# Kernel tuning notes

Hardware: AMD Instinct MI355X
Metric: run time of the kernel (lower is better)

## Reference

```python
import jax, jax.numpy as jnp
import numpy as np

B, CIN, L = 16, 256, 2048
HID, G, M = 512, 2, 512
LP = L // 2  # pooled length == hidden_length of patterns
BETA = 1.0


def setup_inputs() -> dict:
    key = jax.random.key(0)
    k = jax.random.split(key, 6)
    x = jax.random.normal(k[0], (B, CIN, L), dtype=jnp.float32)
    # ChannelPool: Conv1d(256 -> 512, kernel=1, groups=2): weight [512, 128, 1]
    w1 = jax.random.normal(k[1], (HID, CIN // G, 1), dtype=jnp.float32) * 0.05
    b1 = jax.random.normal(k[2], (HID,), dtype=jnp.float32) * 0.01
    # StatePattern memory bank: [num_memories, hidden_length]
    patterns = jax.random.normal(k[3], (M, LP), dtype=jnp.float32) * 0.02
    # Unpool: ConvTranspose1d(512 -> 256, kernel=2, stride=2, groups=2):
    # torch weight layout [in_channels, out_channels//groups, kernel] = [512, 128, 2]
    wT = jax.random.normal(k[4], (HID, CIN // G, 2), dtype=jnp.float32) * 0.05
    bT = jax.random.normal(k[5], (CIN,), dtype=jnp.float32) * 0.01
    RZ = jnp.array(0.1, dtype=jnp.float32)
    return {"x": x, "w1": w1, "b1": b1, "patterns": patterns, "wT": wT, "bT": bT, "RZ": RZ}


def reference(x, w1, b1, patterns, wT, bT, RZ):
    identity = x
    # --- grouped 1x1 conv (ChannelPool) ---
    # split channels into G groups: x [B,G,CIN/G,L], w [G,HID/G,CIN/G]
    xg = x.reshape(B, G, CIN // G, L)
    wg = w1[:, :, 0].reshape(G, HID // G, CIN // G)
    h = jnp.einsum('bgil,goi->bgol', xg, wg).reshape(B, HID, L) + b1[None, :, None]
    h = jax.nn.relu(h)  # act; norm1/dropout are identity (norm=False, eval)
    # --- MaxPool1d(kernel=2, stride=2) ---
    h = h.reshape(B, HID, LP, 2).max(axis=-1)  # [B, HID, LP]
    # --- Hopfield retrieval: softmax(beta * x @ P^T) @ P ---
    scores = jnp.einsum('bcl,ml->bcm', BETA * h, patterns)  # [B, HID, M]
    attn = jax.nn.softmax(scores, axis=-1)
    h = jnp.einsum('bcm,ml->bcl', attn, patterns)  # [B, HID, LP]
    # --- grouped ConvTranspose1d(k=2, s=2) ---
    hg = h.reshape(B, G, HID // G, LP)
    wtg = wT.reshape(G, HID // G, CIN // G, 2)
    y = jnp.einsum('bgil,giok->bgolk', hg, wtg)  # [B,G,CIN/G,LP,2]
    y = y.reshape(B, CIN, L) + bT[None, :, None]
    y = jax.nn.relu(y)  # act; norm2/dropout identity
    return identity + RZ * y
```

## Files before the change

### kernel.cpp

```cpp
#include <hip/hip_runtime.h>

#define NB 16
#define NCIN 256
#define NL 2048
#define NHID 512
#define NM 512
#define NLP 1024
#define BK 64

typedef short bf16x8 __attribute__((ext_vector_type(8)));
typedef unsigned short u16x8 __attribute__((ext_vector_type(8)));
typedef float f32x4 __attribute__((ext_vector_type(4)));
typedef __attribute__((address_space(1))) const unsigned int gas_u32;
typedef __attribute__((address_space(3))) unsigned int las_u32;

__device__ __forceinline__ unsigned short f2bf(float f) {
    unsigned int u = __builtin_bit_cast(unsigned int, f);
    return (unsigned short)((u + 0x7FFFu + ((u >> 16) & 1u)) >> 16);
}
__device__ __forceinline__ float bf2f(unsigned short u) {
    return __builtin_bit_cast(float, ((unsigned int)u) << 16);
}

__global__ __launch_bounds__(256) void k_prep(
    const float* __restrict__ P, const float* __restrict__ w1,
    const float* __restrict__ wT, unsigned short* __restrict__ Pb,
    unsigned short* __restrict__ Ptb, unsigned short* __restrict__ w1b,
    unsigned short* __restrict__ wTt)
{
    __shared__ unsigned short tbuf[64][65];
    const int bb = blockIdx.x;
    if (bb < 128) {
        const int mt = bb >> 4;
        const int lt = bb & 15;
        for (int i = threadIdx.x; i < 4096; i += 256) {
            const int r = i >> 6, c = i & 63;
            const unsigned short b = f2bf(P[(size_t)(mt * 64 + r) * 1024 + lt * 64 + c]);
            Pb[(size_t)(mt * 64 + r) * 1024 + lt * 64 + c] = b;
            tbuf[c][r] = b;
        }
        __syncthreads();
        for (int i = threadIdx.x; i < 4096; i += 256) {
            const int r = i >> 6, c = i & 63;
            Ptb[(size_t)(lt * 64 + r) * 512 + mt * 64 + c] = tbuf[r][c];
        }
    } else {
        const int t = (bb - 128) * 256 + threadIdx.x;
        if (t < 65536) w1b[t] = f2bf(w1[t]);
        if (t < 131072) {
            const int g = t >> 16, ok = (t >> 8) & 255, i = t & 255;
            wTt[t] = f2bf(wT[((size_t)(g * 256 + i)) * 256 + ok]);
        }
    }
}

__global__ __launch_bounds__(256) void k0_xT(
    const float* __restrict__ x, unsigned short* __restrict__ xT)
{
    const int ct = blockIdx.x & 3;
    const int lt = (blockIdx.x >> 2) & 31;
    const int b  = blockIdx.x >> 7;
    __shared__ float tile[64 * 68];
    const int t = threadIdx.x;
    #pragma unroll
    for (int it = 0; it < 4; ++it) {
        const int idx = t + it * 256;
        const int ch = idx >> 4, f4 = idx & 15;
        const float4 v = *(const float4*)(x + ((size_t)(b * 256 + ct * 64 + ch)) * 2048 + lt * 64 + f4 * 4);
        *(float4*)(tile + ch * 68 + f4 * 4) = v;
    }
    __syncthreads();
    const int l = t >> 2, cq = t & 3;
    u16x8 o0, o1;
    #pragma unroll
    for (int k = 0; k < 8; ++k) o0[k] = f2bf(tile[(cq * 16 + k) * 68 + l]);
    #pragma unroll
    for (int k = 0; k < 8; ++k) o1[k] = f2bf(tile[(cq * 16 + 8 + k) * 68 + l]);
    unsigned short* dst = xT + ((size_t)(b * 2048 + lt * 64 + l)) * 256 + ct * 64 + cq * 16;
    *(u16x8*)dst = o0;
    *(u16x8*)(dst + 8) = o1;
}

__global__ __launch_bounds__(256) void k1_gemm(
    const unsigned short* __restrict__ xT, const unsigned short* __restrict__ w1b,
    const float* __restrict__ b1, unsigned short* __restrict__ h)
{
    const int nt = blockIdx.x & 1;
    const int g  = (blockIdx.x >> 1) & 1;
    const int rt = blockIdx.x >> 2;
    const int r0 = rt * 128;
    const int b  = r0 >> 11, l0 = r0 & 2047;
    const int c0 = g * 256 + nt * 128;

    __shared__ unsigned short Asl[128 * BK];
    __shared__ unsigned short Bsl[128 * BK];
    __shared__ unsigned short epi[128 * 72];

    const int t = threadIdx.x;
    const int lane = t & 63;
    const int wave = t >> 6;
    const int wm = wave & 1, wn = wave >> 1;
    const int q = lane >> 4, lm = lane & 15;

    f32x4 acc[4][4];
    #pragma unroll
    for (int i = 0; i < 4; ++i)
        #pragma unroll
        for (int j = 0; j < 4; ++j)
            #pragma unroll
            for (int r = 0; r < 4; ++r) acc[i][j][r] = 0.f;

    for (int k0 = 0; k0 < 128; k0 += BK) {
        #pragma unroll
        for (int rd = 0; rd < 4; ++rd) {
            const int e = rd * 2048 + t * 8;
            const int row = e >> 6, col = e & 63;
            const unsigned short* ga = xT + (size_t)(r0 + row) * 256 + g * 128 + k0 + col;
            __builtin_amdgcn_global_load_lds((gas_u32*)ga, (las_u32*)(Asl + e), 16, 0, 0);
            const unsigned short* gb = w1b + (size_t)(c0 + row) * 128 + k0 + col;
            __builtin_amdgcn_global_load_lds((gas_u32*)gb, (las_u32*)(Bsl + e), 16, 0, 0);
        }
        __syncthreads();
        #pragma unroll
        for (int kk = 0; kk < 2; ++kk) {
            bf16x8 af[4], bf[4];
            #pragma unroll
            for (int i = 0; i < 4; ++i)
                af[i] = *(const bf16x8*)(Asl + (wm * 64 + i * 16 + lm) * BK + kk * 32 + q * 8);
            #pragma unroll
            for (int j = 0; j < 4; ++j)
                bf[j] = *(const bf16x8*)(Bsl + (wn * 64 + j * 16 + lm) * BK + kk * 32 + q * 8);
            #pragma unroll
            for (int i = 0; i < 4; ++i)
                #pragma unroll
                for (int j = 0; j < 4; ++j)
                    acc[i][j] = __builtin_amdgcn_mfma_f32_16x16x32_bf16(af[i], bf[j], acc[i][j], 0, 0, 0);
        }
        __syncthreads();
    }

    #pragma unroll
    for (int j = 0; j < 4; ++j) {
        const int c_blk = wn * 64 + j * 16 + lm;
        const float bias = b1[c0 + c_blk];
        #pragma unroll
        for (int i = 0; i < 4; ++i) {
            const float p0 = fmaxf(fmaxf(acc[i][j][0], acc[i][j][1]) + bias, 0.f);
            const float p1 = fmaxf(fmaxf(acc[i][j][2], acc[i][j][3]) + bias, 0.f);
            const int lp_blk = wm * 32 + i * 8 + q * 2;
            ushort2 u; u.x = f2bf(p0); u.y = f2bf(p1);
            *(ushort2*)(epi + c_blk * 72 + lp_blk) = u;
        }
    }
    __syncthreads();
    const int c_blk = t >> 1, half = t & 1;
    unsigned short* dst = h + ((size_t)(b * 512 + c0 + c_blk)) * 1024 + (l0 >> 1) + half * 32;
    #pragma unroll
    for (int u = 0; u < 4; ++u)
        *(u16x8*)(dst + u * 8) = *(const u16x8*)(epi + c_blk * 72 + half * 32 + u * 8);
}

__global__ __launch_bounds__(512, 2) void gemm_sc(
    const unsigned short* __restrict__ A, const unsigned short* __restrict__ B,
    unsigned short* __restrict__ Sb)
{
    const int nt = blockIdx.x & 3;
    const int rt = blockIdx.x >> 2;
    const int r0 = rt * 128, n0 = nt * 128;

    __shared__ unsigned short Asl[128 * BK];
    __shared__ unsigned short Bsl[128 * BK];

    const int t = threadIdx.x;
    const int lane = t & 63;
    const int wave = t >> 6;
    const int wm = wave & 1, wn = wave >> 1;
    const int q = lane >> 4, lm = lane & 15;

    f32x4 acc[4][2];
    #pragma unroll
    for (int i = 0; i < 4; ++i)
        #pragma unroll
        for (int j = 0; j < 2; ++j)
            #pragma unroll
            for (int r = 0; r < 4; ++r) acc[i][j][r] = 0.f;

    for (int k0 = 0; k0 < 1024; k0 += BK) {
        #pragma unroll
        for (int rd = 0; rd < 2; ++rd) {
            const int e = rd * 4096 + t * 8;
            const int row = e >> 6, col = e & 63;
            const unsigned short* ga = A + (size_t)(r0 + row) * 1024 + k0 + col;
            __builtin_amdgcn_global_load_lds((gas_u32*)ga, (las_u32*)(Asl + e), 16, 0, 0);
            const unsigned short* gb = B + (size_t)(n0 + row) * 1024 + k0 + col;
            __builtin_amdgcn_global_load_lds((gas_u32*)gb, (las_u32*)(Bsl + e), 16, 0, 0);
        }
        __syncthreads();
        #pragma unroll
        for (int kk = 0; kk < 2; ++kk) {
            bf16x8 af[4], bf[2];
            #pragma unroll
            for (int i = 0; i < 4; ++i)
                af[i] = *(const bf16x8*)(Asl + (wm * 64 + i * 16 + lm) * BK + kk * 32 + q * 8);
            #pragma unroll
            for (int j = 0; j < 2; ++j)
                bf[j] = *(const bf16x8*)(Bsl + (wn * 32 + j * 16 + lm) * BK + kk * 32 + q * 8);
            #pragma unroll
            for (int i = 0; i < 4; ++i)
                #pragma unroll
                for (int j = 0; j < 2; ++j)
                    acc[i][j] = __builtin_amdgcn_mfma_f32_16x16x32_bf16(af[i], bf[j], acc[i][j], 0, 0, 0);
        }
        __syncthreads();
    }

    #pragma unroll
    for (int i = 0; i < 4; ++i)
        #pragma unroll
        for (int j = 0; j < 2; ++j)
            #pragma unroll
            for (int r = 0; r < 4; ++r)
                Sb[(size_t)(r0 + wm * 64 + i * 16 + q * 4 + r) * 512
                   + n0 + wn * 32 + j * 16 + lm] = f2bf(acc[i][j][r]);
}

__global__ __launch_bounds__(256) void k_softmax(
    const unsigned short* __restrict__ Sb, unsigned short* __restrict__ Ab)
{
    const int row = blockIdx.x * 4 + (threadIdx.x >> 6);
    const int lane = threadIdx.x & 63;
    const u16x8 uv = *(const u16x8*)(Sb + (size_t)row * 512 + lane * 8);

    float v[8];
    #pragma unroll
    for (int j = 0; j < 8; ++j) v[j] = bf2f(uv[j]);

    float mx = v[0];
    #pragma unroll
    for (int j = 1; j < 8; ++j) mx = fmaxf(mx, v[j]);
    for (int off = 32; off > 0; off >>= 1) mx = fmaxf(mx, __shfl_xor(mx, off));

    float sum = 0.f;
    #pragma unroll
    for (int j = 0; j < 8; ++j) { v[j] = __expf(v[j] - mx); sum += v[j]; }
    for (int off = 32; off > 0; off >>= 1) sum += __shfl_xor(sum, off);

    const float inv = 1.f / sum;
    u16x8 ov;
    #pragma unroll
    for (int j = 0; j < 8; ++j) ov[j] = f2bf(v[j] * inv);
    *(u16x8*)(Ab + (size_t)row * 512 + lane * 8) = ov;
}

__global__ __launch_bounds__(512, 4) void gemm_retr(
    const unsigned short* __restrict__ Ptb, const unsigned short* __restrict__ Ab,
    unsigned short* __restrict__ h2T)
{
    const int tl = blockIdx.x & 31;
    const int b  = blockIdx.x >> 5;
    const int nt = tl & 3;
    const int rt = tl >> 2;
    const int r0 = rt * 128, n0 = nt * 128;

    __shared__ unsigned short Asl[128 * BK];
    __shared__ unsigned short Bsl[128 * BK];

    const int t = threadIdx.x;
    const int lane = t & 63;
    const int wave = t >> 6;
    const int wm = wave & 1, wn = wave >> 1;
    const int q = lane >> 4, lm = lane & 15;

    f32x4 acc[4][2];
    #pragma unroll
    for (int i = 0; i < 4; ++i)
        #pragma unroll
        for (int j = 0; j < 2; ++j)
            #pragma unroll
            for (int r = 0; r < 4; ++r) acc[i][j][r] = 0.f;

    for (int k0 = 0; k0 < 512; k0 += BK) {
        #pragma unroll
        for (int rd = 0; rd < 2; ++rd) {
            const int e = rd * 4096 + t * 8;
            const int row = e >> 6, col = e & 63;
            const unsigned short* ga = Ptb + (size_t)(r0 + row) * 512 + k0 + col;
            __builtin_amdgcn_global_load_lds((gas_u32*)ga, (las_u32*)(Asl + e), 16, 0, 0);
            const unsigned short* gb = Ab + ((size_t)b * 512 + n0 + row) * 512 + k0 + col;
            __builtin_amdgcn_global_load_lds((gas_u32*)gb, (las_u32*)(Bsl + e), 16, 0, 0);
        }
        __syncthreads();
        #pragma unroll
        for (int kk = 0; kk < 2; ++kk) {
            bf16x8 af[4], bf[2];
            #pragma unroll
            for (int i = 0; i < 4; ++i)
                af[i] = *(const bf16x8*)(Asl + (wm * 64 + i * 16 + lm) * BK + kk * 32 + q * 8);
            #pragma unroll
            for (int j = 0; j < 2; ++j)
                bf[j] = *(const bf16x8*)(Bsl + (wn * 32 + j * 16 + lm) * BK + kk * 32 + q * 8);
            #pragma unroll
            for (int i = 0; i < 4; ++i)
                #pragma unroll
                for (int j = 0; j < 2; ++j)
                    acc[i][j] = __builtin_amdgcn_mfma_f32_16x16x32_bf16(af[i], bf[j], acc[i][j], 0, 0, 0);
        }
        __syncthreads();
    }

    #pragma unroll
    for (int i = 0; i < 4; ++i)
        #pragma unroll
        for (int j = 0; j < 2; ++j)
            #pragma unroll
            for (int r = 0; r < 4; ++r)
                h2T[((size_t)b * 1024 + r0 + wm * 64 + i * 16 + q * 4 + r) * 512
                    + n0 + wn * 32 + j * 16 + lm] = f2bf(acc[i][j][r]);
}

__global__ __launch_bounds__(256) void k4_gemm(
    const unsigned short* __restrict__ h2T, const unsigned short* __restrict__ wTt,
    const float* __restrict__ bT, const float* __restrict__ x,
    const float* __restrict__ RZ, float* __restrict__ out)
{
    const int nt = blockIdx.x & 1;
    const int g  = (blockIdx.x >> 1) & 1;
    const int rt = blockIdx.x >> 2;
    const int r0 = rt * 128;
    const int b  = r0 >> 10, lp0 = r0 & 1023;

    __shared__ __align__(16) char smem[65536];
    unsigned short* Asl = (unsigned short*)smem;
    unsigned short* Bsl = Asl + 128 * BK;
    float* epi = (float*)smem;

    const int t = threadIdx.x;
    const int lane = t & 63;
    const int wave = t >> 6;
    const int wm = wave & 1, wn = wave >> 1;
    const int q = lane >> 4, lm = lane & 15;

    f32x4 acc[4][4];
    #pragma unroll
    for (int i = 0; i < 4; ++i)
        #pragma unroll
        for (int j = 0; j < 4; ++j)
            #pragma unroll
            for (int r = 0; r < 4; ++r) acc[i][j][r] = 0.f;

    for (int k0 = 0; k0 < 256; k0 += BK) {
        #pragma unroll
        for (int rd = 0; rd < 4; ++rd) {
            const int e = rd * 2048 + t * 8;
            const int row = e >> 6, col = e & 63;
            const unsigned short* ga = h2T + (size_t)(r0 + row) * 512 + g * 256 + k0 + col;
            __builtin_amdgcn_global_load_lds((gas_u32*)ga, (las_u32*)(Asl + e), 16, 0, 0);
            const unsigned short* gb = wTt + (size_t)g * 65536 + (size_t)(nt * 128 + row) * 256 + k0 + col;
            __builtin_amdgcn_global_load_lds((gas_u32*)gb, (las_u32*)(Bsl + e), 16, 0, 0);
        }
        __syncthreads();
        #pragma unroll
        for (int kk = 0; kk < 2; ++kk) {
            bf16x8 af[4], bf[4];
            #pragma unroll
            for (int i = 0; i < 4; ++i)
                af[i] = *(const bf16x8*)(Asl + (wm * 64 + i * 16 + lm) * BK + kk * 32 + q * 8);
            #pragma unroll
            for (int j = 0; j < 4; ++j)
                bf[j] = *(const bf16x8*)(Bsl + (wn * 64 + j * 16 + lm) * BK + kk * 32 + q * 8);
            #pragma unroll
            for (int i = 0; i < 4; ++i)
                #pragma unroll
                for (int j = 0; j < 4; ++j)
                    acc[i][j] = __builtin_amdgcn_mfma_f32_16x16x32_bf16(af[i], bf[j], acc[i][j], 0, 0, 0);
        }
        __syncthreads();
    }

    #pragma unroll
    for (int j = 0; j < 4; ++j) {
        const int col_blk = wn * 64 + j * 16 + lm;
        const int o_l = col_blk >> 1, kk2 = col_blk & 1;
        #pragma unroll
        for (int i = 0; i < 4; ++i) {
            #pragma unroll
            for (int r = 0; r < 4; ++r) {
                const int row_l = wm * 64 + i * 16 + q * 4 + r;
                const int l_l = 2 * row_l + kk2;
                const int chunk = ((l_l >> 2) + o_l) & 63;
                epi[o_l * 256 + chunk * 4 + (l_l & 3)] = acc[i][j][r];
            }
        }
    }
    __syncthreads();
    const int row = t >> 2, quad = t & 3;
    const int c = g * 128 + nt * 64 + row;
    const float bias = bT[c];
    const float rz = RZ[0];
    const size_t gbase = ((size_t)(b * 256 + c)) * 2048 + 2 * lp0 + quad * 64;
    #pragma unroll
    for (int k = 0; k < 16; ++k) {
        const int chunk_phys = (quad * 16 + k + row) & 63;
        const float4 v = *(const float4*)(epi + row * 256 + chunk_phys * 4);
        const float4 xv = *(const float4*)(x + gbase + k * 4);
        float4 o;
        o.x = xv.x + rz * fmaxf(v.x + bias, 0.f);
        o.y = xv.y + rz * fmaxf(v.y + bias, 0.f);
        o.z = xv.z + rz * fmaxf(v.z + bias, 0.f);
        o.w = xv.w + rz * fmaxf(v.w + bias, 0.f);
        *(float4*)(out + gbase + k * 4) = o;
    }
}

extern "C" void kernel_launch(void* const* d_in, const int* in_sizes, int n_in,
                              void* d_out, int out_size, void* d_ws, size_t ws_size,
                              hipStream_t stream) {
    (void)in_sizes; (void)n_in; (void)out_size; (void)ws_size;
    const float* x  = (const float*)d_in[0];
    const float* w1 = (const float*)d_in[1];
    const float* b1 = (const float*)d_in[2];
    const float* P  = (const float*)d_in[3];
    const float* wT = (const float*)d_in[4];
    const float* bT = (const float*)d_in[5];
    const float* RZ = (const float*)d_in[6];
    float* out = (float*)d_out;

    char* ws = (char*)d_ws;
    unsigned short* xT  = (unsigned short*)ws;
    unsigned short* h2T = (unsigned short*)ws;
    unsigned short* hb  = (unsigned short*)(ws + (16u << 20));
    unsigned short* Ab  = (unsigned short*)(ws + (16u << 20));
    unsigned short* Pb  = (unsigned short*)(ws + (32u << 20));
    unsigned short* Ptb = (unsigned short*)(ws + (33u << 20));
    unsigned short* w1b = (unsigned short*)(ws + (34u << 20));
    unsigned short* wTt = (unsigned short*)(ws + (34u << 20) + (256u << 10));
    unsigned short* Sb  = (unsigned short*)out;

    hipLaunchKernelGGL(k_prep,    dim3(640),  dim3(256), 0, stream, P, w1, wT, Pb, Ptb, w1b, wTt);
    hipLaunchKernelGGL(k0_xT,     dim3(2048), dim3(256), 0, stream, x, xT);
    hipLaunchKernelGGL(k1_gemm,   dim3(1024), dim3(256), 0, stream, xT, w1b, b1, hb);
    hipLaunchKernelGGL(gemm_sc,   dim3(256),  dim3(512), 0, stream, hb, Pb, Sb);
    hipLaunchKernelGGL(k_softmax, dim3(2048), dim3(256), 0, stream, Sb, Ab);
    hipLaunchKernelGGL(gemm_retr, dim3(512),  dim3(512), 0, stream, Ptb, Ab, h2T);
    hipLaunchKernelGGL(k4_gemm,   dim3(512),  dim3(256), 0, stream, h2T, wTt, bT, x, RZ, out);
}
```

Baseline: 186.9 us.

## Fuse front-end conv and Hopfield score/softmax/retrieval into fewer kernels

Collapses seven launches into three. The first kernel merges weight prep, the x transpose/bf16 conversion and the grouped 1x1 conv into one launch. The second computes scores, softmax and retrieval for a 32-row tile entirely in LDS, so the score matrix is never written to or read back from global memory. The aim is to remove intermediate global traffic and launch gaps, at the cost of fewer blocks in the Hopfield stage (256) and big LDS footprints that limit occupancy. The patterns matrix is also reloaded by every block.

```diff
diff --git a/kernel.cpp b/kernel.cpp
--- a/kernel.cpp
+++ b/kernel.cpp
@@ -6,7 +6,6 @@
 #define NHID 512
 #define NM 512
 #define NLP 1024
-#define BK 64
 
 typedef short bf16x8 __attribute__((ext_vector_type(8)));
 typedef unsigned short u16x8 __attribute__((ext_vector_type(8)));
@@ -22,83 +21,82 @@
     return __builtin_bit_cast(float, ((unsigned int)u) << 16);
 }
 
-__global__ __launch_bounds__(256) void k_prep(
-    const float* __restrict__ P, const float* __restrict__ w1,
-    const float* __restrict__ wT, unsigned short* __restrict__ Pb,
-    unsigned short* __restrict__ Ptb, unsigned short* __restrict__ w1b,
+__global__ __launch_bounds__(512) void k_front(
+    const float* __restrict__ x, const float* __restrict__ w1,
+    const float* __restrict__ b1, const float* __restrict__ P,
+    const float* __restrict__ wT, unsigned short* __restrict__ hb,
+    unsigned short* __restrict__ Pb, unsigned short* __restrict__ Ptb,
     unsigned short* __restrict__ wTt)
 {
-    __shared__ unsigned short tbuf[64][65];
+    __shared__ __align__(16) unsigned short smem[66560];
     const int bb = blockIdx.x;
-    if (bb < 128) {
-        const int mt = bb >> 4;
-        const int lt = bb & 15;
-        for (int i = threadIdx.x; i < 4096; i += 256) {
-            const int r = i >> 6, c = i & 63;
-            const unsigned short b = f2bf(P[(size_t)(mt * 64 + r) * 1024 + lt * 64 + c]);
-            Pb[(size_t)(mt * 64 + r) * 1024 + lt * 64 + c] = b;
-            tbuf[c][r] = b;
-        }
-        __syncthreads();
-        for (int i = threadIdx.x; i < 4096; i += 256) {
-            const int r = i >> 6, c = i & 63;
-            Ptb[(size_t)(lt * 64 + r) * 512 + mt * 64 + c] = tbuf[r][c];
-        }
-    } else {
-        const int t = (bb - 128) * 256 + threadIdx.x;
-        if (t < 65536) w1b[t] = f2bf(w1[t]);
-        if (t < 131072) {
-            const int g = t >> 16, ok = (t >> 8) & 255, i = t & 255;
-            wTt[t] = f2bf(wT[((size_t)(g * 256 + i)) * 256 + ok]);
-        }
-    }
-}
-
-__global__ __launch_bounds__(256) void k0_xT(
-    const float* __restrict__ x, unsigned short* __restrict__ xT)
-{
-    const int ct = blockIdx.x & 3;
-    const int lt = (blockIdx.x >> 2) & 31;
-    const int b  = blockIdx.x >> 7;
-    __shared__ float tile[64 * 68];
     const int t = threadIdx.x;
-    #pragma unroll
-    for (int it = 0; it < 4; ++it) {
-        const int idx = t + it * 256;
-        const int ch = idx >> 4, f4 = idx & 15;
-        const float4 v = *(const float4*)(x + ((size_t)(b * 256 + ct * 64 + ch)) * 2048 + lt * 64 + f4 * 4);
-        *(float4*)(tile + ch * 68 + f4 * 4) = v;
-    }
-    __syncthreads();
-    const int l = t >> 2, cq = t & 3;
-    u16x8 o0, o1;
-    #pragma unroll
-    for (int k = 0; k < 8; ++k) o0[k] = f2bf(tile[(cq * 16 + k) * 68 + l]);
-    #pragma unroll
-    for (int k = 0; k < 8; ++k) o1[k] = f2bf(tile[(cq * 16 + 8 + k) * 68 + l]);
-    unsigned short* dst = xT + ((size_t)(b * 2048 + lt * 64 + l)) * 256 + ct * 64 + cq * 16;
-    *(u16x8*)dst = o0;
-    *(u16x8*)(dst + 8) = o1;
-}
-
-__global__ __launch_bounds__(256) void k1_gemm(
-    const unsigned short* __restrict__ xT, const unsigned short* __restrict__ w1b,
-    const float* __restrict__ b1, unsigned short* __restrict__ h)
-{
-    const int nt = blockIdx.x & 1;
-    const int g  = (blockIdx.x >> 1) & 1;
-    const int rt = blockIdx.x >> 2;
+
+    if (bb >= 512) {
+        if (bb < 640) {
+            unsigned short (*tbuf)[65] = (unsigned short (*)[65])smem;
+            const int pb = bb - 512;
+            const int mt = pb >> 4, lt = pb & 15;
+            for (int i = t; i < 4096; i += 512) {
+                const int r = i >> 6, c = i & 63;
+                const unsigned short v = f2bf(P[(size_t)(mt * 64 + r) * 1024 + lt * 64 + c]);
+                Pb[(size_t)(mt * 64 + r) * 1024 + lt * 64 + c] = v;
+                tbuf[c][r] = v;
+            }
+            __syncthreads();
+            for (int i = t; i < 4096; i += 512) {
+                const int r = i >> 6, c = i & 63;
+                Ptb[(size_t)(lt * 64 + r) * 512 + mt * 64 + c] = tbuf[r][c];
+            }
+        } else {
+            const int t5 = (bb - 640) * 512 + t;
+            const int g = t5 >> 16, ok = (t5 >> 8) & 255, i = t5 & 255;
+            wTt[t5] = f2bf(wT[(size_t)(g * 256 + i) * 256 + ok]);
+        }
+        return;
+    }
+
+    const int g  = bb & 1;
+    const int rt = bb >> 1;
     const int r0 = rt * 128;
     const int b  = r0 >> 11, l0 = r0 & 2047;
-    const int c0 = g * 256 + nt * 128;
-
-    __shared__ unsigned short Asl[128 * BK];
-    __shared__ unsigned short Bsl[128 * BK];
-    __shared__ unsigned short epi[128 * 72];
-
-    const int t = threadIdx.x;
-    const int lane = t & 63;
-    const int wave = t >> 6;
+
+    unsigned short* T   = smem;
+    unsigned short* Asl = smem + 17408;
+    unsigned short* Bsl = smem + 33792;
+    unsigned short* epi = smem;
+
+    #pragma unroll
+    for (int i3 = 0; i3 < 8; ++i3) {
+        const int idx = i3 * 512 + t;
+        const int ch = idx >> 5, f4 = idx & 31;
+        const float4 v = *(const float4*)(x + ((size_t)(b * 256 + g * 128 + ch)) * 2048 + l0 + f4 * 4);
+        ushort4 u;
+        u.x = f2bf(v.x); u.y = f2bf(v.y); u.z = f2bf(v.z); u.w = f2bf(v.w);
+        *(ushort4*)(T + ch * 136 + f4 * 4) = u;
+    }
+    #pragma unroll
+    for (int i5 = 0; i5 < 16; ++i5) {
+        const int idx = i5 * 512 + t;
+        const int o = idx >> 5, f4 = idx & 31;
+        const float4 v = *(const float4*)(w1 + ((size_t)(g * 256 + o)) * 128 + f4 * 4);
+        ushort4 u;
+        u.x = f2bf(v.x); u.y = f2bf(v.y); u.z = f2bf(v.z); u.w = f2bf(v.w);
+        *(ushort4*)(Bsl + o * 128 + f4 * 4) = u;
+    }
+    __syncthreads();
+    #pragma unroll
+    for (int i4 = 0; i4 < 4; ++i4) {
+        const int idx = i4 * 512 + t;
+        const int ch = idx & 127, lo = idx >> 7;
+        const u16x8 v = *(const u16x8*)(T + ch * 136 + lo * 8);
+        #pragma unroll
+        for (int u2 = 0; u2 < 8; ++u2)
+            Asl[(lo * 8 + u2) * 128 + ch] = v[u2];
+    }
+    __syncthreads();
+
+    const int lane = t & 63, wave = t >> 6;
     const int wm = wave & 1, wn = wave >> 1;
     const int q = lane >> 4, lm = lane & 15;
 
@@ -110,212 +108,197 @@
             #pragma unroll
             for (int r = 0; r < 4; ++r) acc[i][j][r] = 0.f;
 
-    for (int k0 = 0; k0 < 128; k0 += BK) {
-        #pragma unroll
-        for (int rd = 0; rd < 4; ++rd) {
-            const int e = rd * 2048 + t * 8;
-            const int row = e >> 6, col = e & 63;
-            const unsigned short* ga = xT + (size_t)(r0 + row) * 256 + g * 128 + k0 + col;
-            __builtin_amdgcn_global_load_lds((gas_u32*)ga, (las_u32*)(Asl + e), 16, 0, 0);
-            const unsigned short* gb = w1b + (size_t)(c0 + row) * 128 + k0 + col;
-            __builtin_amdgcn_global_load_lds((gas_u32*)gb, (las_u32*)(Bsl + e), 16, 0, 0);
-        }
-        __syncthreads();
-        #pragma unroll
-        for (int kk = 0; kk < 2; ++kk) {
-            bf16x8 af[4], bf[4];
-            #pragma unroll
-            for (int i = 0; i < 4; ++i)
-                af[i] = *(const bf16x8*)(Asl + (wm * 64 + i * 16 + lm) * BK + kk * 32 + q * 8);
+    #pragma unroll
+    for (int kc = 0; kc < 4; ++kc) {
+        bf16x8 af[4], bf[4];
+        #pragma unroll
+        for (int i = 0; i < 4; ++i)
+            af[i] = *(const bf16x8*)(Asl + (wm * 64 + i * 16 + lm) * 128 + kc * 32 + q * 8);
+        #pragma unroll
+        for (int j = 0; j < 4; ++j)
+            bf[j] = *(const bf16x8*)(Bsl + (wn * 64 + j * 16 + lm) * 128 + kc * 32 + q * 8);
+        #pragma unroll
+        for (int i = 0; i < 4; ++i)
             #pragma unroll
             for (int j = 0; j < 4; ++j)
-                bf[j] = *(const bf16x8*)(Bsl + (wn * 64 + j * 16 + lm) * BK + kk * 32 + q * 8);
-            #pragma unroll
-            for (int i = 0; i < 4; ++i)
-                #pragma unroll
-                for (int j = 0; j < 4; ++j)
-                    acc[i][j] = __builtin_amdgcn_mfma_f32_16x16x32_bf16(af[i], bf[j], acc[i][j], 0, 0, 0);
-        }
-        __syncthreads();
-    }
+                acc[i][j] = __builtin_amdgcn_mfma_f32_16x16x32_bf16(af[i], bf[j], acc[i][j], 0, 0, 0);
+    }
+    __syncthreads();
 
     #pragma unroll
     for (int j = 0; j < 4; ++j) {
-        const int c_blk = wn * 64 + j * 16 + lm;
-        const float bias = b1[c0 + c_blk];
+        const int col = wn * 64 + j * 16 + lm;
+        const float bias = b1[g * 256 + col];
         #pragma unroll
         for (int i = 0; i < 4; ++i) {
             const float p0 = fmaxf(fmaxf(acc[i][j][0], acc[i][j][1]) + bias, 0.f);
             const float p1 = fmaxf(fmaxf(acc[i][j][2], acc[i][j][3]) + bias, 0.f);
-            const int lp_blk = wm * 32 + i * 8 + q * 2;
+            const int lp_loc = wm * 32 + i * 8 + q * 2;
             ushort2 u; u.x = f2bf(p0); u.y = f2bf(p1);
-            *(ushort2*)(epi + c_blk * 72 + lp_blk) = u;
-        }
-    }
-    __syncthreads();
-    const int c_blk = t >> 1, half = t & 1;
-    unsigned short* dst = h + ((size_t)(b * 512 + c0 + c_blk)) * 1024 + (l0 >> 1) + half * 32;
+            *(ushort2*)(epi + col * 72 + lp_loc) = u;
+        }
+    }
+    __syncthreads();
+    const int c_loc = t >> 1, half = t & 1;
+    unsigned short* dst = hb + ((size_t)(b * 512 + g * 256 + c_loc)) * 1024 + (l0 >> 1) + half * 32;
     #pragma unroll
     for (int u = 0; u < 4; ++u)
-        *(u16x8*)(dst + u * 8) = *(const u16x8*)(epi + c_blk * 72 + half * 32 + u * 8);
-}
-
-__global__ __launch_bounds__(512, 2) void gemm_sc(
-    const unsigned short* __restrict__ A, const unsigned short* __restrict__ B,
-    unsigned short* __restrict__ Sb)
+        *(u16x8*)(dst + u * 8) = *(const u16x8*)(epi + c_loc * 72 + half * 32 + u * 8);
+}
+
+__global__ __launch_bounds__(512) void k_hop(
+    const unsigned short* __restrict__ hb, const unsigned short* __restrict__ Pb,
+    const unsigned short* __restrict__ Ptb, unsigned short* __restrict__ h2T)
 {
-    const int nt = blockIdx.x & 3;
-    const int rt = blockIdx.x >> 2;
-    const int r0 = rt * 128, n0 = nt * 128;
-
-    __shared__ unsigned short Asl[128 * BK];
-    __shared__ unsigned short Bsl[128 * BK];
+    __shared__ __align__(16) unsigned short smem[51712];
+    unsigned short* Sbuf = smem;
+    unsigned short* Asl  = smem + 16896;
+    unsigned short* Bsl  = smem + 16896 + 2048;
+    unsigned short* Bsl2 = smem + 16896;
 
     const int t = threadIdx.x;
-    const int lane = t & 63;
-    const int wave = t >> 6;
-    const int wm = wave & 1, wn = wave >> 1;
+    const int r0 = blockIdx.x * 32;
+    const int b = r0 >> 9, c0 = r0 & 511;
+    const int lane = t & 63, wave = t >> 6;
     const int q = lane >> 4, lm = lane & 15;
 
-    f32x4 acc[4][2];
-    #pragma unroll
-    for (int i = 0; i < 4; ++i)
-        #pragma unroll
-        for (int j = 0; j < 2; ++j)
-            #pragma unroll
-            for (int r = 0; r < 4; ++r) acc[i][j][r] = 0.f;
-
-    for (int k0 = 0; k0 < 1024; k0 += BK) {
-        #pragma unroll
-        for (int rd = 0; rd < 2; ++rd) {
-            const int e = rd * 4096 + t * 8;
+    f32x4 acc1[2][4];
+    #pragma unroll
+    for (int i = 0; i < 2; ++i)
+        #pragma unroll
+        for (int j = 0; j < 4; ++j)
+            #pragma unroll
+            for (int r = 0; r < 4; ++r) acc1[i][j][r] = 0.f;
+
+    for (int kc0 = 0; kc0 < 1024; kc0 += 64) {
+        if (t < 256) {
+            const int e = t * 8;
             const int row = e >> 6, col = e & 63;
-            const unsigned short* ga = A + (size_t)(r0 + row) * 1024 + k0 + col;
+            const unsigned short* ga = hb + (size_t)(r0 + row) * 1024 + kc0 + col;
             __builtin_amdgcn_global_load_lds((gas_u32*)ga, (las_u32*)(Asl + e), 16, 0, 0);
-            const unsigned short* gb = B + (size_t)(n0 + row) * 1024 + k0 + col;
+        }
+        #pragma unroll
+        for (int i2 = 0; i2 < 8; ++i2) {
+            const int e = (i2 * 512 + t) * 8;
+            const int row = e >> 6, col = e & 63;
+            const unsigned short* gb = Pb + (size_t)row * 1024 + kc0 + col;
             __builtin_amdgcn_global_load_lds((gas_u32*)gb, (las_u32*)(Bsl + e), 16, 0, 0);
         }
         __syncthreads();
         #pragma unroll
         for (int kk = 0; kk < 2; ++kk) {
-            bf16x8 af[4], bf[2];
-            #pragma unroll
-            for (int i = 0; i < 4; ++i)
-                af[i] = *(const bf16x8*)(Asl + (wm * 64 + i * 16 + lm) * BK + kk * 32 + q * 8);
+            bf16x8 af[2], bf[4];
+            #pragma unroll
+            for (int i = 0; i < 2; ++i)
+                af[i] = *(const bf16x8*)(Asl + (i * 16 + lm) * 64 + kk * 32 + q * 8);
+            #pragma unroll
+            for (int j = 0; j < 4; ++j)
+                bf[j] = *(const bf16x8*)(Bsl + (wave * 64 + j * 16 + lm) * 64 + kk * 32 + q * 8);
+            #pragma unroll
+            for (int i = 0; i < 2; ++i)
+                #pragma unroll
+                for (int j = 0; j < 4; ++j)
+                    acc1[i][j] = __builtin_amdgcn_mfma_f32_16x16x32_bf16(af[i], bf[j], acc1[i][j], 0, 0, 0);
+        }
+        __syncthreads();
+    }
+
+    #pragma unroll
+    for (int i = 0; i < 2; ++i)
+        #pragma unroll
+        for (int j = 0; j < 4; ++j)
+            #pragma unroll
+            for (int r = 0; r < 4; ++r)
+                Sbuf[(i * 16 + q * 4 + r) * 528 + wave * 64 + j * 16 + lm] = f2bf(acc1[i][j][r]);
+    __syncthreads();
+
+    {
+        const int rw = t >> 4, sl = t & 15;
+        u16x8 sv[4];
+        #pragma unroll
+        for (int u = 0; u < 4; ++u)
+            sv[u] = *(const u16x8*)(Sbuf + rw * 528 + sl * 32 + u * 8);
+        float mx = -3.0e38f;
+        #pragma unroll
+        for (int u = 0; u < 4; ++u)
+            #pragma unroll
+            for (int j = 0; j < 8; ++j) mx = fmaxf(mx, bf2f(sv[u][j]));
+        #pragma unroll
+        for (int off = 1; off < 16; off <<= 1) mx = fmaxf(mx, __shfl_xor(mx, off));
+        float vv[32];
+        float sum = 0.f;
+        #pragma unroll
+        for (int u = 0; u < 4; ++u)
+            #pragma unroll
+            for (int j = 0; j < 8; ++j) {
+                const float e = __expf(bf2f(sv[u][j]) - mx);
+                vv[u * 8 + j] = e; sum += e;
+            }
+        #pragma unroll
+        for (int off = 1; off < 16; off <<= 1) sum += __shfl_xor(sum, off);
+        const float inv = 1.f / sum;
+        #pragma unroll
+        for (int u = 0; u < 4; ++u) {
+            u16x8 ov;
+            #pragma unroll
+            for (int j = 0; j < 8; ++j) ov[j] = f2bf(vv[u * 8 + j] * inv);
+            *(u16x8*)(Sbuf + rw * 528 + sl * 32 + u * 8) = ov;
+        }
+    }
+    __syncthreads();
+
+    bf16x8 a[2][16];
+    #pragma unroll
+    for (int i = 0; i < 2; ++i)
+        #pragma unroll
+        for (int kx = 0; kx < 16; ++kx)
+            a[i][kx] = *(const bf16x8*)(Sbuf + (i * 16 + lm) * 528 + kx * 32 + q * 8);
+
+    for (int lpc = 0; lpc < 4; ++lpc) {
+        const int lp0c = lpc * 256;
+        f32x4 acc2[2][2];
+        #pragma unroll
+        for (int i = 0; i < 2; ++i)
             #pragma unroll
             for (int j = 0; j < 2; ++j)
-                bf[j] = *(const bf16x8*)(Bsl + (wn * 32 + j * 16 + lm) * BK + kk * 32 + q * 8);
-            #pragma unroll
-            for (int i = 0; i < 4; ++i)
+                #pragma unroll
+                for (int r = 0; r < 4; ++r) acc2[i][j][r] = 0.f;
+
+        for (int kc0 = 0; kc0 < 4; ++kc0) {
+            #pragma unroll
+            for (int i2 = 0; i2 < 8; ++i2) {
+                const int e = (i2 * 512 + t) * 8;
+                const int row = e >> 7, col = e & 127;
+                const unsigned short* gb = Ptb + (size_t)(lp0c + row) * 512 + kc0 * 128 + col;
+                __builtin_amdgcn_global_load_lds((gas_u32*)gb, (las_u32*)(Bsl2 + e), 16, 0, 0);
+            }
+            __syncthreads();
+            #pragma unroll
+            for (int kk = 0; kk < 4; ++kk) {
+                const int kx = kc0 * 4 + kk;
+                bf16x8 bf2[2];
                 #pragma unroll
                 for (int j = 0; j < 2; ++j)
-                    acc[i][j] = __builtin_amdgcn_mfma_f32_16x16x32_bf16(af[i], bf[j], acc[i][j], 0, 0, 0);
-        }
-        __syncthreads();
-    }
-
-    #pragma unroll
-    for (int i = 0; i < 4; ++i)
-        #pragma unroll
-        for (int j = 0; j < 2; ++j)
-            #pragma unroll
-            for (int r = 0; r < 4; ++r)
-                Sb[(size_t)(r0 + wm * 64 + i * 16 + q * 4 + r) * 512
-                   + n0 + wn * 32 + j * 16 + lm] = f2bf(acc[i][j][r]);
-}
-
-__global__ __launch_bounds__(256) void k_softmax(
-    const unsigned short* __restrict__ Sb, unsigned short* __restrict__ Ab)
-{
-    const int row = blockIdx.x * 4 + (threadIdx.x >> 6);
-    const int lane = threadIdx.x & 63;
-    const u16x8 uv = *(const u16x8*)(Sb + (size_t)row * 512 + lane * 8);
-
-    float v[8];
-    #pragma unroll
-    for (int j = 0; j < 8; ++j) v[j] = bf2f(uv[j]);
-
-    float mx = v[0];
-    #pragma unroll
-    for (int j = 1; j < 8; ++j) mx = fmaxf(mx, v[j]);
-    for (int off = 32; off > 0; off >>= 1) mx = fmaxf(mx, __shfl_xor(mx, off));
-
-    float sum = 0.f;
-    #pragma unroll
-    for (int j = 0; j < 8; ++j) { v[j] = __expf(v[j] - mx); sum += v[j]; }
-    for (int off = 32; off > 0; off >>= 1) sum += __shfl_xor(sum, off);
-
-    const float inv = 1.f / sum;
-    u16x8 ov;
-    #pragma unroll
-    for (int j = 0; j < 8; ++j) ov[j] = f2bf(v[j] * inv);
-    *(u16x8*)(Ab + (size_t)row * 512 + lane * 8) = ov;
-}
-
-__global__ __launch_bounds__(512, 4) void gemm_retr(
-    const unsigned short* __restrict__ Ptb, const unsigned short* __restrict__ Ab,
-    unsigned short* __restrict__ h2T)
-{
-    const int tl = blockIdx.x & 31;
-    const int b  = blockIdx.x >> 5;
-    const int nt = tl & 3;
-    const int rt = tl >> 2;
-    const int r0 = rt * 128, n0 = nt * 128;
-
-    __shared__ unsigned short Asl[128 * BK];
-    __shared__ unsigned short Bsl[128 * BK];
-
-    const int t = threadIdx.x;
-    const int lane = t & 63;
-    const int wave = t >> 6;
-    const int wm = wave & 1, wn = wave >> 1;
-    const int q = lane >> 4, lm = lane & 15;
-
-    f32x4 acc[4][2];
-    #pragma unroll
-    for (int i = 0; i < 4; ++i)
-        #pragma unroll
-        for (int j = 0; j < 2; ++j)
-            #pragma unroll
-            for (int r = 0; r < 4; ++r) acc[i][j][r] = 0.f;
-
-    for (int k0 = 0; k0 < 512; k0 += BK) {
-        #pragma unroll
-        for (int rd = 0; rd < 2; ++rd) {
-            const int e = rd * 4096 + t * 8;
-            const int row = e >> 6, col = e & 63;
-            const unsigned short* ga = Ptb + (size_t)(r0 + row) * 512 + k0 + col;
-            __builtin_amdgcn_global_load_lds((gas_u32*)ga, (las_u32*)(Asl + e), 16, 0, 0);
-            const unsigned short* gb = Ab + ((size_t)b * 512 + n0 + row) * 512 + k0 + col;
-            __builtin_amdgcn_global_load_lds((gas_u32*)gb, (las_u32*)(Bsl + e), 16, 0, 0);
-        }
-        __syncthreads();
-        #pragma unroll
-        for (int kk = 0; kk < 2; ++kk) {
-            bf16x8 af[4], bf[2];
-            #pragma unroll
-            for (int i = 0; i < 4; ++i)
-                af[i] = *(const bf16x8*)(Asl + (wm * 64 + i * 16 + lm) * BK + kk * 32 + q * 8);
-            #pragma unroll
-            for (int j = 0; j < 2; ++j)
-                bf[j] = *(const bf16x8*)(Bsl + (wn * 32 + j * 16 + lm) * BK + kk * 32 + q * 8);
-            #pragma unroll
-            for (int i = 0; i < 4; ++i)
+                    bf2[j] = *(const bf16x8*)(Bsl2 + (wave * 32 + j * 16 + lm) * 128 + kk * 32 + q * 8);
                 #pragma unroll
-                for (int j = 0; j < 2; ++j)
-                    acc[i][j] = __builtin_amdgcn_mfma_f32_16x16x32_bf16(af[i], bf[j], acc[i][j], 0, 0, 0);
-        }
-        __syncthreads();
-    }
-
-    #pragma unroll
-    for (int i = 0; i < 4; ++i)
-        #pragma unroll
-        for (int j = 0; j < 2; ++j)
-            #pragma unroll
-            for (int r = 0; r < 4; ++r)
-                h2T[((size_t)b * 1024 + r0 + wm * 64 + i * 16 + q * 4 + r) * 512
-                    + n0 + wn * 32 + j * 16 + lm] = f2bf(acc[i][j][r]);
+                for (int i = 0; i < 2; ++i)
+                    #pragma unroll
+                    for (int j = 0; j < 2; ++j)
+                        acc2[i][j] = __builtin_amdgcn_mfma_f32_16x16x32_bf16(a[i][kx], bf2[j], acc2[i][j], 0, 0, 0);
+            }
+            __syncthreads();
+        }
+        #pragma unroll
+        for (int i = 0; i < 2; ++i)
+            #pragma unroll
+            for (int j = 0; j < 2; ++j) {
+                const int lp = lp0c + wave * 32 + j * 16 + lm;
+                ushort4 u;
+                u.x = f2bf(acc2[i][j][0]); u.y = f2bf(acc2[i][j][1]);
+                u.z = f2bf(acc2[i][j][2]); u.w = f2bf(acc2[i][j][3]);
+                *(ushort4*)(h2T + ((size_t)b * 1024 + lp) * 512 + c0 + i * 16 + q * 4) = u;
+            }
+    }
 }
 
 __global__ __launch_bounds__(256) void k4_gemm(
@@ -331,7 +314,7 @@
 
     __shared__ __align__(16) char smem[65536];
     unsigned short* Asl = (unsigned short*)smem;
-    unsigned short* Bsl = Asl + 128 * BK;
+    unsigned short* Bsl = Asl + 128 * 64;
     float* epi = (float*)smem;
 
     const int t = threadIdx.x;
@@ -348,7 +331,7 @@
             #pragma unroll
             for (int r = 0; r < 4; ++r) acc[i][j][r] = 0.f;
 
-    for (int k0 = 0; k0 < 256; k0 += BK) {
+    for (int k0 = 0; k0 < 256; k0 += 64) {
         #pragma unroll
         for (int rd = 0; rd < 4; ++rd) {
             const int e = rd * 2048 + t * 8;
@@ -364,10 +347,10 @@
             bf16x8 af[4], bf[4];
             #pragma unroll
             for (int i = 0; i < 4; ++i)
-                af[i] = *(const bf16x8*)(Asl + (wm * 64 + i * 16 + lm) * BK + kk * 32 + q * 8);
+                af[i] = *(const bf16x8*)(Asl + (wm * 64 + i * 16 + lm) * 64 + kk * 32 + q * 8);
             #pragma unroll
             for (int j = 0; j < 4; ++j)
-                bf[j] = *(const bf16x8*)(Bsl + (wn * 64 + j * 16 + lm) * BK + kk * 32 + q * 8);
+                bf[j] = *(const bf16x8*)(Bsl + (wn * 64 + j * 16 + lm) * 64 + kk * 32 + q * 8);
             #pragma unroll
             for (int i = 0; i < 4; ++i)
                 #pragma unroll
@@ -426,21 +409,14 @@
     float* out = (float*)d_out;
 
     char* ws = (char*)d_ws;
-    unsigned short* xT  = (unsigned short*)ws;
-    unsigned short* h2T = (unsigned short*)ws;
-    unsigned short* hb  = (unsigned short*)(ws + (16u << 20));
-    unsigned short* Ab  = (unsigned short*)(ws + (16u << 20));
+    unsigned short* hb  = (unsigned short*)ws;
+    unsigned short* h2T = (unsigned short*)(ws + (16u << 20));
     unsigned short* Pb  = (unsigned short*)(ws + (32u << 20));
     unsigned short* Ptb = (unsigned short*)(ws + (33u << 20));
-    unsigned short* w1b = (unsigned short*)(ws + (34u << 20));
-    unsigned short* wTt = (unsigned short*)(ws + (34u << 20) + (256u << 10));
-    unsigned short* Sb  = (unsigned short*)out;
-
-    hipLaunchKernelGGL(k_prep,    dim3(640),  dim3(256), 0, stream, P, w1, wT, Pb, Ptb, w1b, wTt);
-    hipLaunchKernelGGL(k0_xT,     dim3(2048), dim3(256), 0, stream, x, xT);
-    hipLaunchKernelGGL(k1_gemm,   dim3(1024), dim3(256), 0, stream, xT, w1b, b1, hb);
-    hipLaunchKernelGGL(gemm_sc,   dim3(256),  dim3(512), 0, stream, hb, Pb, Sb);
-    hipLaunchKernelGGL(k_softmax, dim3(2048), dim3(256), 0, stream, Sb, Ab);
-    hipLaunchKernelGGL(gemm_retr, dim3(512),  dim3(512), 0, stream, Ptb, Ab, h2T);
-    hipLaunchKernelGGL(k4_gemm,   dim3(512),  dim3(256), 0, stream, h2T, wTt, bT, x, RZ, out);
-}
+    unsigned short* wTt = (unsigned short*)(ws + (34u << 20));
+
+    hipLaunchKernelGGL(k_front, dim3(896), dim3(512), 0, stream,
+                       x, w1, b1, P, wT, hb, Pb, Ptb, wTt);
+    hipLaunchKernelGGL(k_hop,   dim3(256), dim3(512), 0, stream, hb, Pb, Ptb, h2T);
+    hipLaunchKernelGGL(k4_gemm, dim3(512), dim3(256), 0, stream, h2T, wTt, bT, x, RZ, out);
+}
```

New measurement: 201.2 us. 1.08x slower.
